# Kernel tuning notes

Hardware: AMD Instinct MI355X
Metric: run time of the kernel (lower is better)

The kernel has to match this reference:

```python
import jax, jax.numpy as jnp
import numpy as np

B, S, D, H, DFF = 4, 2048, 1024, 16, 4096
DK = D // H
EPS = 1e-5


def _linear_params(key, fan_in, fan_out):
    kw, kb = jax.random.split(key)
    bound = 1.0 / np.sqrt(fan_in)
    w = jax.random.uniform(kw, (fan_in, fan_out), minval=-bound, maxval=bound, dtype=jnp.float32)
    b = jax.random.uniform(kb, (fan_out,), minval=-bound, maxval=bound, dtype=jnp.float32)
    return w, b


def setup_inputs() -> dict:
    key = jax.random.key(0)
    ks = jax.random.split(key, 8)
    x = jax.random.normal(ks[0], (B, S, D), dtype=jnp.float32)
    mask = jnp.ones((B, 1, 1, S), dtype=jnp.int32)
    wq, bq = _linear_params(ks[1], D, D)
    wk, bk = _linear_params(ks[2], D, D)
    wv, bv = _linear_params(ks[3], D, D)
    wo, bo = _linear_params(ks[4], D, D)
    w1, b1 = _linear_params(ks[5], D, DFF)
    w2, b2 = _linear_params(ks[6], DFF, D)
    g1 = jnp.ones((D,), jnp.float32); be1 = jnp.zeros((D,), jnp.float32)
    g2 = jnp.ones((D,), jnp.float32); be2 = jnp.zeros((D,), jnp.float32)
    return {"x": x, "mask": mask, "wq": wq, "bq": bq, "wk": wk, "bk": bk,
            "wv": wv, "bv": bv, "wo": wo, "bo": bo, "w1": w1, "b1": b1,
            "w2": w2, "b2": b2, "g1": g1, "be1": be1, "g2": g2, "be2": be2}


def _layernorm(x, g, b):
    mu = jnp.mean(x, axis=-1, keepdims=True)
    var = jnp.mean(jnp.square(x - mu), axis=-1, keepdims=True)
    return (x - mu) * jax.lax.rsqrt(var + EPS) * g + b


def reference(x, mask, wq, bq, wk, bk, wv, bv, wo, bo, w1, b1, w2, b2, g1, be1, g2, be2):
    # Multi-head self-attention
    q = (x @ wq + bq).reshape(B, S, H, DK).transpose(0, 2, 1, 3)  # b h s d
    k = (x @ wk + bk).reshape(B, S, H, DK).transpose(0, 2, 1, 3)
    v = (x @ wv + bv).reshape(B, S, H, DK).transpose(0, 2, 1, 3)
    scores = jnp.einsum('bhqd,bhkd->bhqk', q, k) / np.sqrt(DK)
    scores = jnp.where(mask == 0, jnp.float32(-1e9), scores)
    attn = jax.nn.softmax(scores, axis=-1)
    ctx = jnp.einsum('bhqk,bhkd->bhqd', attn, v)
    ctx = ctx.transpose(0, 2, 1, 3).reshape(B, S, D)
    attn_out = ctx @ wo + bo
    # Dropout is identity in eval mode
    out1 = _layernorm(x + attn_out, g1, be1)
    ffn = jax.nn.relu(out1 @ w1 + b1) @ w2 + b2
    out2 = _layernorm(out1 + ffn, g2, be2)
    return out2
```

## Files before the change

### kernel.cpp

```cpp
#include <hip/hip_runtime.h>
#include <cstdint>
#include <cstddef>

typedef __bf16 bf16_t;
typedef __bf16 bf16x4 __attribute__((ext_vector_type(4)));
typedef __bf16 bf16x8 __attribute__((ext_vector_type(8)));
typedef float f32x4 __attribute__((ext_vector_type(4)));

#define GLD_LDS16(g, l)                                                                   \
  __builtin_amdgcn_global_load_lds((const __attribute__((address_space(1))) void*)(g),   \
                                   (__attribute__((address_space(3))) void*)(l), 16, 0, 0)

__device__ __forceinline__ int swbits(int row) {
  return ((row ^ (row >> 3)) & 7) << 4;
}
__device__ __forceinline__ int swz(int row, int colbyte) {
  return row * 128 + (colbyte ^ swbits(row));
}

__global__ __launch_bounds__(256) void transpose_cvt_k(const float* __restrict__ src,
                                                       bf16_t* __restrict__ dst, int R, int C) {
  __shared__ float t[64][65];
  const int tid = threadIdx.x;
  const int tr = blockIdx.y * 64, tc = blockIdx.x * 64;
  const int r0 = tid >> 2, c0 = (tid & 3) * 16;
#pragma unroll
  for (int i = 0; i < 16; i += 4) {
    float4 v = *(const float4*)(src + (size_t)(tr + r0) * C + tc + c0 + i);
    t[r0][c0 + i] = v.x; t[r0][c0 + i + 1] = v.y;
    t[r0][c0 + i + 2] = v.z; t[r0][c0 + i + 3] = v.w;
  }
  __syncthreads();
  bf16x8 w0, w1;
#pragma unroll
  for (int i = 0; i < 8; ++i) {
    w0[i] = (bf16_t)t[c0 + i][r0];
    w1[i] = (bf16_t)t[c0 + 8 + i][r0];
  }
  *(bf16x8*)(dst + (size_t)(tc + r0) * R + tr + c0) = w0;
  *(bf16x8*)(dst + (size_t)(tc + r0) * R + tr + c0 + 8) = w1;
}

__global__ __launch_bounds__(256) void cvt_k(const float* __restrict__ in,
                                             bf16_t* __restrict__ out) {
  const size_t i = ((size_t)blockIdx.x * 256 + threadIdx.x) * 8;
  float4 a = *(const float4*)(in + i);
  float4 b = *(const float4*)(in + i + 4);
  bf16x8 o;
  o[0] = (bf16_t)a.x; o[1] = (bf16_t)a.y; o[2] = (bf16_t)a.z; o[3] = (bf16_t)a.w;
  o[4] = (bf16_t)b.x; o[5] = (bf16_t)b.y; o[6] = (bf16_t)b.z; o[7] = (bf16_t)b.w;
  *(bf16x8*)(out + i) = o;
}

__global__ void mask_scan_k(const int* __restrict__ mask, unsigned* __restrict__ dirty) {
  __shared__ int tilez[32];
  const int tid = threadIdx.x;
  for (int b = 0; b < 4; ++b) {
    if (tid < 32) tilez[tid] = 0;
    __syncthreads();
    int anyz = 0;
    const int* mb = mask + b * 2048 + tid * 8;
#pragma unroll
    for (int j = 0; j < 8; ++j) anyz |= (mb[j] == 0);
    if (anyz) atomicOr(&tilez[tid >> 3], 1);
    __syncthreads();
    if (tid == 0) {
      unsigned w = 0;
      for (int k = 0; k < 32; ++k) w |= (tilez[k] ? 1u : 0u) << k;
      dirty[b] = w;
    }
    __syncthreads();
  }
}

template <int EPI>
__global__ __launch_bounds__(256) void gemm_bt(
    const bf16_t* __restrict__ A, const bf16_t* __restrict__ Bt,
    const float* __restrict__ bias0, const bf16_t* __restrict__ res,
    bf16_t* __restrict__ out0, int N, int K) {
  __shared__ __align__(16) bf16_t As[128][64];
  __shared__ __align__(16) bf16_t Bs[128][64];
  const int tid = threadIdx.x, lane = tid & 63, wave = tid >> 6;
  const int wm = wave >> 1, wn = wave & 1;
  const int tile_m = blockIdx.y * 128, tile_n = blockIdx.x * 128;

  f32x4 acc[4][4];
#pragma unroll
  for (int i = 0; i < 4; ++i)
#pragma unroll
    for (int j = 0; j < 4; ++j)
#pragma unroll
      for (int c = 0; c < 4; ++c) acc[i][j][c] = 0.f;

  for (int k0 = 0; k0 < K; k0 += 64) {
    __syncthreads();
#pragma unroll
    for (int j = 0; j < 4; ++j) {
      const int c = j * 256 + tid;
      GLD_LDS16(A + (size_t)(tile_m + (c >> 3)) * K + k0 + (c & 7) * 8,
                (char*)As + j * 4096 + wave * 1024);
      GLD_LDS16(Bt + (size_t)(tile_n + (c >> 3)) * K + k0 + (c & 7) * 8,
                (char*)Bs + j * 4096 + wave * 1024);
    }
    __syncthreads();
#pragma unroll
    for (int kk = 0; kk < 2; ++kk) {
      bf16x8 a[4], b[4];
#pragma unroll
      for (int i = 0; i < 4; ++i)
        a[i] = *(const bf16x8*)&As[wm * 64 + i * 16 + (lane & 15)][kk * 32 + (lane >> 4) * 8];
#pragma unroll
      for (int i = 0; i < 4; ++i)
        b[i] = *(const bf16x8*)&Bs[wn * 64 + i * 16 + (lane & 15)][kk * 32 + (lane >> 4) * 8];
#pragma unroll
      for (int mi = 0; mi < 4; ++mi)
#pragma unroll
        for (int ni = 0; ni < 4; ++ni)
          acc[mi][ni] = __builtin_amdgcn_mfma_f32_16x16x32_bf16(a[mi], b[ni], acc[mi][ni], 0, 0, 0);
    }
  }

#pragma unroll
  for (int mi = 0; mi < 4; ++mi) {
#pragma unroll
    for (int ni = 0; ni < 4; ++ni) {
      const int col = tile_n + wn * 64 + ni * 16 + (lane & 15);
      const int rbase = tile_m + wm * 64 + mi * 16 + (lane >> 4) * 4;
      const float bv = bias0[col];
#pragma unroll
      for (int r = 0; r < 4; ++r) {
        const int row = rbase + r;
        float v = acc[mi][ni][r] + bv;
        if constexpr (EPI == 1) v += (float)res[(size_t)row * N + col];
        out0[(size_t)row * N + col] = (bf16_t)v;
      }
    }
  }
}

template <int EPI>
__global__ __launch_bounds__(512, 1) void gemm256(
    const bf16_t* __restrict__ A, const bf16_t* __restrict__ Bt,
    const float* __restrict__ bias0, const float* __restrict__ bias1,
    const float* __restrict__ bias2,
    bf16_t* __restrict__ out0, bf16_t* __restrict__ out1, bf16_t* __restrict__ out2,
    int N, int K) {
  extern __shared__ __align__(16) char lds[];
  const int tid = threadIdx.x, lane = tid & 63, wave = tid >> 6;
  const int fr = lane & 15, hi = lane >> 4;
  const int wm = wave >> 2, wn = wave & 3;
  const int tile_n = blockIdx.x * 256, tile_m = blockIdx.y * 256;
  const int NT = K >> 6;
  const int s_r = tid >> 3, s_cb = (tid & 7) * 16;

  f32x4 acc[8][4];
#pragma unroll
  for (int m = 0; m < 8; ++m)
#pragma unroll
    for (int n = 0; n < 4; ++n)
#pragma unroll
      for (int c = 0; c < 4; ++c) acc[m][n][c] = 0.f;

#define STAGE256(t, cbuf)                                                                  \
  do {                                                                                     \
    const size_t k0_ = (size_t)(t) * 64;                                                   \
    _Pragma("unroll") for (int h_ = 0; h_ < 2; ++h_)                                       \
        _Pragma("unroll") for (int is_ = 0; is_ < 2; ++is_) {                              \
      const int r_ = is_ * 64 + s_r;                                                       \
      GLD_LDS16(A + (size_t)(tile_m + h_ * 128 + r_) * K + k0_ + ((s_cb ^ swbits(r_)) >> 1),\
                lds + (cbuf)*65536 + h_ * 16384 + is_ * 8192 + wave * 1024);               \
    }                                                                                      \
    _Pragma("unroll") for (int h_ = 0; h_ < 2; ++h_)                                       \
        _Pragma("unroll") for (int is_ = 0; is_ < 2; ++is_) {                              \
      const int r_ = is_ * 64 + s_r;                                                       \
      GLD_LDS16(Bt + (size_t)(tile_n + h_ * 128 + r_) * K + k0_ + ((s_cb ^ swbits(r_)) >> 1),\
                lds + (cbuf)*65536 + 32768 + h_ * 16384 + is_ * 8192 + wave * 1024);       \
    }                                                                                      \
  } while (0)

  STAGE256(0, 0);
  for (int t = 0; t < NT; ++t) {
    const int c = t & 1;
    if (t + 1 < NT) {
      STAGE256(t + 1, c ^ 1);
      asm volatile("s_waitcnt vmcnt(8)" ::: "memory");
    } else {
      asm volatile("s_waitcnt vmcnt(0)" ::: "memory");
    }
    __builtin_amdgcn_s_barrier();

    bf16x8 bfrag[4][2];
#pragma unroll
    for (int n = 0; n < 4; ++n)
#pragma unroll
      for (int kk = 0; kk < 2; ++kk)
        bfrag[n][kk] = *(const bf16x8*)(lds + c * 65536 + 32768 + (wn >> 1) * 16384 +
                                        swz((wn & 1) * 64 + n * 16 + fr, kk * 64 + hi * 16));
    bf16x8 af[2][2][2];
#pragma unroll
    for (int mm = 0; mm < 2; ++mm)
#pragma unroll
      for (int kk = 0; kk < 2; ++kk)
        af[0][mm][kk] = *(const bf16x8*)(lds + c * 65536 + wm * 16384 +
                                         swz(mm * 16 + fr, kk * 64 + hi * 16));
#pragma unroll
    for (int p = 0; p < 4; ++p) {
      if (p < 3) {
#pragma unroll
        for (int mm = 0; mm < 2; ++mm)
#pragma unroll
          for (int kk = 0; kk < 2; ++kk)
            af[(p + 1) & 1][mm][kk] =
                *(const bf16x8*)(lds + c * 65536 + wm * 16384 +
                                 swz(((p + 1) * 2 + mm) * 16 + fr, kk * 64 + hi * 16));
      }
      __builtin_amdgcn_s_setprio(1);
#pragma unroll
      for (int mm = 0; mm < 2; ++mm)
#pragma unroll
        for (int n = 0; n < 4; ++n)
#pragma unroll
          for (int kk = 0; kk < 2; ++kk)
            acc[p * 2 + mm][n] = __builtin_amdgcn_mfma_f32_16x16x32_bf16(
                af[p & 1][mm][kk], bfrag[n][kk], acc[p * 2 + mm][n], 0, 0, 0);
      __builtin_amdgcn_s_setprio(0);
    }
    __builtin_amdgcn_s_barrier();
  }
#undef STAGE256

#pragma unroll
  for (int m = 0; m < 8; ++m) {
#pragma unroll
    for (int n = 0; n < 4; ++n) {
      const int col = tile_n + wn * 64 + n * 16 + fr;
      const int rbase = tile_m + wm * 128 + m * 16 + hi * 4;
      if constexpr (EPI == 0) {
        const int which = tile_n >> 10;
        const float* bp = which == 0 ? bias0 : (which == 1 ? bias1 : bias2);
        bf16_t* op = which == 0 ? out0 : (which == 1 ? out1 : out2);
        const float sca = which == 0 ? 0.18033688f : 1.0f;
        const int cc = col & 1023, h = cc >> 6, dk = cc & 63;
        const float bv = bp[cc];
#pragma unroll
        for (int r = 0; r < 4; ++r) {
          const int row = rbase + r, bb = row >> 11, ss = row & 2047;
          op[(((size_t)bb * 16 + h) * 2048 + ss) * 64 + dk] = (bf16_t)((acc[m][n][r] + bv) * sca);
        }
      } else {
        const float bv = bias0[col];
#pragma unroll
        for (int r = 0; r < 4; ++r) {
          const int row = rbase + r;
          float v = acc[m][n][r] + bv;
          if constexpr (EPI == 2) v = v > 0.f ? v : 0.f;
          out0[(size_t)row * N + col] = (bf16_t)v;
        }
      }
    }
  }
}

__global__ __launch_bounds__(256) void attn_k(
    const bf16_t* __restrict__ Q, const bf16_t* __restrict__ Kb, const bf16_t* __restrict__ Vb,
    const int* __restrict__ mask, const unsigned* __restrict__ dirtyp,
    bf16_t* __restrict__ ctxout) {
  __shared__ __align__(16) char Qs[16384];
  __shared__ __align__(16) char Ks[2][8192];
  __shared__ __align__(16) char Vt[2][8192];
  __shared__ __align__(16) char Ps[16384];
  const int tid = threadIdx.x, lane = tid & 63, wave = tid >> 6;
  const int fr = lane & 15, hi = lane >> 4;
  const int qt = blockIdx.x, bh = blockIdx.y, b = bh >> 4, h = bh & 15;
  const bf16_t* qbase = Q + ((size_t)bh * 2048 + qt * 128) * 64;
  const bf16_t* kbase = Kb + (size_t)bh * 2048 * 64;
  const bf16_t* vbase = Vb + (size_t)bh * 2048 * 64;
  const int* mbase = mask + b * 2048;
  const unsigned dirty = dirtyp[b];

  const int src_r = tid >> 3;
  const int src_cb = (tid & 7) * 16;

#pragma unroll
  for (int j = 0; j < 4; ++j) {
    const int c = j * 256 + tid, rr = c >> 3, cb = (c & 7) * 16;
    GLD_LDS16(qbase + rr * 64 + ((cb ^ swbits(rr)) >> 1), Qs + j * 4096 + wave * 1024);
  }
#pragma unroll
  for (int j = 0; j < 2; ++j) {
    const int rr = j * 32 + src_r;
    GLD_LDS16(kbase + rr * 64 + ((src_cb ^ swbits(rr)) >> 1), Ks[0] + j * 4096 + wave * 1024);
  }
  {
    bf16x8 v0 = *(const bf16x8*)(vbase + (size_t)(tid >> 3) * 64 + (tid & 7) * 8);
    bf16x8 v1 = *(const bf16x8*)(vbase + (size_t)(32 + (tid >> 3)) * 64 + (tid & 7) * 8);
    const int kp0 = tid >> 3, kp1 = 32 + (tid >> 3), d0 = (tid & 7) * 8;
#pragma unroll
    for (int i = 0; i < 8; ++i) {
      *(bf16_t*)(Vt[0] + swz(d0 + i, kp0 * 2)) = v0[i];
      *(bf16_t*)(Vt[0] + swz(d0 + i, kp1 * 2)) = v1[i];
    }
  }
  __syncthreads();

  f32x4 ctx[2][4];
  float l_prt[2][4];
#pragma unroll
  for (int mi = 0; mi < 2; ++mi)
#pragma unroll
    for (int r = 0; r < 4; ++r) {
      l_prt[mi][r] = 0.f;
#pragma unroll
      for (int di = 0; di < 4; ++di) ctx[mi][di][r] = 0.f;
    }

  for (int kt = 0; kt < 32; ++kt) {
    const int cur = kt & 1;
    bf16x8 vr0, vr1;
    if (kt < 31) {
#pragma unroll
      for (int j = 0; j < 2; ++j) {
        const int rr = j * 32 + src_r;
        GLD_LDS16(kbase + (size_t)(kt + 1) * 4096 + rr * 64 + ((src_cb ^ swbits(rr)) >> 1),
                  Ks[cur ^ 1] + j * 4096 + wave * 1024);
      }
      vr0 = *(const bf16x8*)(vbase + (size_t)(kt + 1) * 4096 + (size_t)(tid >> 3) * 64 +
                             (tid & 7) * 8);
      vr1 = *(const bf16x8*)(vbase + (size_t)(kt + 1) * 4096 + (size_t)(32 + (tid >> 3)) * 64 +
                             (tid & 7) * 8);
    }

    f32x4 sc[2][4];
#pragma unroll
    for (int mi = 0; mi < 2; ++mi)
#pragma unroll
      for (int ni = 0; ni < 4; ++ni)
#pragma unroll
        for (int c = 0; c < 4; ++c) sc[mi][ni][c] = 0.f;
#pragma unroll
    for (int kk = 0; kk < 2; ++kk) {
      bf16x8 aq[2], kb_[4];
#pragma unroll
      for (int mi = 0; mi < 2; ++mi)
        aq[mi] = *(const bf16x8*)(Qs + swz(wave * 32 + mi * 16 + fr, kk * 64 + hi * 16));
#pragma unroll
      for (int ni = 0; ni < 4; ++ni)
        kb_[ni] = *(const bf16x8*)(Ks[cur] + swz(ni * 16 + fr, kk * 64 + hi * 16));
#pragma unroll
      for (int mi = 0; mi < 2; ++mi)
#pragma unroll
        for (int ni = 0; ni < 4; ++ni)
          sc[mi][ni] = __builtin_amdgcn_mfma_f32_16x16x32_bf16(aq[mi], kb_[ni], sc[mi][ni], 0, 0, 0);
    }

    if (dirty & (1u << kt)) {
      int mv[4];
#pragma unroll
      for (int ni = 0; ni < 4; ++ni) mv[ni] = mbase[kt * 64 + ni * 16 + fr];
#pragma unroll
      for (int mi = 0; mi < 2; ++mi)
#pragma unroll
        for (int ni = 0; ni < 4; ++ni)
#pragma unroll
          for (int r = 0; r < 4; ++r)
            sc[mi][ni][r] = mv[ni] ? sc[mi][ni][r] : -1e9f;
    }

#pragma unroll
    for (int mi = 0; mi < 2; ++mi) {
#pragma unroll
      for (int r = 0; r < 4; ++r) {
        float rsum = 0.f;
#pragma unroll
        for (int ni = 0; ni < 4; ++ni) {
          const float p = exp2f(sc[mi][ni][r]);
          sc[mi][ni][r] = p;
          rsum += p;
        }
        l_prt[mi][r] += rsum;
      }
      const int qrow = wave * 32 + mi * 16 + hi * 4;
#pragma unroll
      for (int ni = 0; ni < 4; ++ni)
#pragma unroll
        for (int r = 0; r < 4; ++r)
          *(bf16_t*)(Ps + swz(qrow + r, (ni * 16 + fr) * 2)) = (bf16_t)sc[mi][ni][r];
    }
    asm volatile("s_waitcnt lgkmcnt(0)" ::: "memory");
    __builtin_amdgcn_sched_barrier(0);

#pragma unroll
    for (int kk = 0; kk < 2; ++kk) {
      bf16x8 pa[2], vv[4];
#pragma unroll
      for (int mi = 0; mi < 2; ++mi)
        pa[mi] = *(const bf16x8*)(Ps + swz(wave * 32 + mi * 16 + fr, kk * 64 + hi * 16));
#pragma unroll
      for (int di = 0; di < 4; ++di)
        vv[di] = *(const bf16x8*)(Vt[cur] + swz(di * 16 + fr, kk * 64 + hi * 16));
#pragma unroll
      for (int mi = 0; mi < 2; ++mi)
#pragma unroll
        for (int di = 0; di < 4; ++di)
          ctx[mi][di] =
              __builtin_amdgcn_mfma_f32_16x16x32_bf16(pa[mi], vv[di], ctx[mi][di], 0, 0, 0);
    }

    if (kt < 31) {
      const int kp0 = tid >> 3, kp1 = 32 + (tid >> 3), d0 = (tid & 7) * 8;
#pragma unroll
      for (int i = 0; i < 8; ++i) {
        *(bf16_t*)(Vt[cur ^ 1] + swz(d0 + i, kp0 * 2)) = vr0[i];
        *(bf16_t*)(Vt[cur ^ 1] + swz(d0 + i, kp1 * 2)) = vr1[i];
      }
    }
    __syncthreads();
  }

#pragma unroll
  for (int mi = 0; mi < 2; ++mi)
#pragma unroll
    for (int r = 0; r < 4; ++r) {
      float l = l_prt[mi][r];
#pragma unroll
      for (int d = 1; d < 16; d <<= 1) l += __shfl_xor(l, d);
      const float inv = 1.f / l;
      const int srow = qt * 128 + wave * 32 + mi * 16 + hi * 4 + r;
#pragma unroll
      for (int di = 0; di < 4; ++di) {
        const int col = h * 64 + di * 16 + fr;
        ctxout[((size_t)b * 2048 + srow) * 1024 + col] = (bf16_t)(ctx[mi][di][r] * inv);
      }
    }
}

template <int F32OUT>
__global__ __launch_bounds__(256) void ln_k(const bf16_t* __restrict__ in,
                                            const float* __restrict__ g,
                                            const float* __restrict__ be,
                                            void* __restrict__ out) {
  __shared__ float red[8];
  const int tid = threadIdx.x;
  const size_t row = blockIdx.x;
  bf16x4 v4 = *(const bf16x4*)(in + row * 1024 + tid * 4);
  const float f0 = (float)v4[0], f1 = (float)v4[1], f2 = (float)v4[2], f3 = (float)v4[3];
  float s = f0 + f1 + f2 + f3;
  float s2 = f0 * f0 + f1 * f1 + f2 * f2 + f3 * f3;
#pragma unroll
  for (int d = 1; d < 64; d <<= 1) { s += __shfl_xor(s, d); s2 += __shfl_xor(s2, d); }
  if ((tid & 63) == 0) { red[tid >> 6] = s; red[4 + (tid >> 6)] = s2; }
  __syncthreads();
  s = red[0] + red[1] + red[2] + red[3];
  s2 = red[4] + red[5] + red[6] + red[7];
  const float mu = s * (1.f / 1024.f);
  const float var = s2 * (1.f / 1024.f) - mu * mu;
  const float rs = rsqrtf(var + 1e-5f);
  float4 gv = *(const float4*)(g + tid * 4);
  float4 bv = *(const float4*)(be + tid * 4);
  const float r0 = (f0 - mu) * rs * gv.x + bv.x;
  const float r1 = (f1 - mu) * rs * gv.y + bv.y;
  const float r2 = (f2 - mu) * rs * gv.z + bv.z;
  const float r3 = (f3 - mu) * rs * gv.w + bv.w;
  if constexpr (F32OUT) {
    float4 o = {r0, r1, r2, r3};
    *(float4*)((float*)out + row * 1024 + tid * 4) = o;
  } else {
    bf16x4 o;
    o[0] = (bf16_t)r0; o[1] = (bf16_t)r1; o[2] = (bf16_t)r2; o[3] = (bf16_t)r3;
    *(bf16x4*)((bf16_t*)out + row * 1024 + tid * 4) = o;
  }
}

extern "C" void kernel_launch(void* const* d_in, const int* in_sizes, int n_in,
                              void* d_out, int out_size, void* d_ws, size_t ws_size,
                              hipStream_t stream) {
  const float* x    = (const float*)d_in[0];
  const int*   mask = (const int*)d_in[1];
  const float* wq = (const float*)d_in[2];
  const float* bq = (const float*)d_in[3];
  const float* wk = (const float*)d_in[4];
  const float* bk = (const float*)d_in[5];
  const float* wv = (const float*)d_in[6];
  const float* bv = (const float*)d_in[7];
  const float* wo = (const float*)d_in[8];
  const float* bo = (const float*)d_in[9];
  const float* w1 = (const float*)d_in[10];
  const float* b1 = (const float*)d_in[11];
  const float* w2 = (const float*)d_in[12];
  const float* b2 = (const float*)d_in[13];
  const float* g1  = (const float*)d_in[14];
  const float* be1 = (const float*)d_in[15];
  const float* g2  = (const float*)d_in[16];
  const float* be2 = (const float*)d_in[17];

  char* wsb = (char*)d_ws;
  bf16_t* S0  = (bf16_t*)wsb;
  bf16_t* XB  = (bf16_t*)(wsb + 8388608);
  bf16_t* QB  = (bf16_t*)(wsb + 25165824);
  bf16_t* KB  = (bf16_t*)(wsb + 41943040);
  bf16_t* VB  = (bf16_t*)(wsb + 58720256);
  bf16_t* CTX = (bf16_t*)(wsb + 75497472);
  bf16_t* FFN = QB;
  bf16_t* Y   = (bf16_t*)(wsb + 92274688);
  bf16_t* O1  = (bf16_t*)(wsb + 109051904);
  unsigned* DIRTY = (unsigned*)(wsb + 125829120);

  (void)hipFuncSetAttribute((const void*)gemm256<0>,
                            hipFuncAttributeMaxDynamicSharedMemorySize, 131072);
  (void)hipFuncSetAttribute((const void*)gemm256<2>,
                            hipFuncAttributeMaxDynamicSharedMemorySize, 131072);

  dim3 blk(256);
  mask_scan_k<<<1, 256, 0, stream>>>(mask, DIRTY);
  cvt_k<<<4096, blk, 0, stream>>>(x, XB);
  transpose_cvt_k<<<dim3(16, 16), blk, 0, stream>>>(wq, S0, 1024, 1024);
  transpose_cvt_k<<<dim3(16, 16), blk, 0, stream>>>(wk, S0 + 1048576, 1024, 1024);
  transpose_cvt_k<<<dim3(16, 16), blk, 0, stream>>>(wv, S0 + 2097152, 1024, 1024);
  gemm256<0><<<dim3(12, 32), 512, 131072, stream>>>(XB, S0, bq, bk, bv,
                                                    QB, KB, VB, 3072, 1024);
  transpose_cvt_k<<<dim3(16, 16), blk, 0, stream>>>(wo, S0, 1024, 1024);
  attn_k<<<dim3(16, 64), blk, 0, stream>>>(QB, KB, VB, mask, DIRTY, CTX);
  gemm_bt<1><<<dim3(8, 64), blk, 0, stream>>>(CTX, S0, bo, XB, Y, 1024, 1024);
  transpose_cvt_k<<<dim3(64, 16), blk, 0, stream>>>(w1, S0, 1024, 4096);
  ln_k<0><<<8192, blk, 0, stream>>>(Y, g1, be1, O1);
  gemm256<2><<<dim3(16, 32), 512, 131072, stream>>>(O1, S0, b1, nullptr, nullptr,
                                                    FFN, nullptr, nullptr, 4096, 1024);
  transpose_cvt_k<<<dim3(16, 64), blk, 0, stream>>>(w2, S0, 4096, 1024);
  gemm_bt<1><<<dim3(8, 64), blk, 0, stream>>>(FFN, S0, b2, O1, Y, 1024, 4096);
  ln_k<1><<<8192, blk, 0, stream>>>(Y, g2, be2, d_out);
}
```

Before: 487.7 us.

## Add double-buffered 256x128 swizzled GEMM for QKV, out-proj and FFN2

Replaces the simple single-buffered 128x128 gemm_bt with a new 512-thread 256x128-tile kernel that double-buffers LDS, uses an XOR swizzle and issues next-tile loads before the MFMA work. The new kernel now serves the output projection and FFN2 GEMMs (N=1024), and also the QKV projection, which moves off the 256x256 kernel to get more blocks (768 instead of 384). The aim is to hide global-load latency, cut LDS bank conflicts, and fill the CUs better for the narrower GEMMs. The cost is that the smaller tile gives less data reuse per block than the 256x256 kernel, and the larger LDS footprint (96KB) allows only one block per CU.

```diff
diff --git a/kernel.cpp b/kernel.cpp
--- a/kernel.cpp
+++ b/kernel.cpp
@@ -74,65 +74,117 @@
 }
 
 template <int EPI>
-__global__ __launch_bounds__(256) void gemm_bt(
+__global__ __launch_bounds__(512, 1) void gemmA(
     const bf16_t* __restrict__ A, const bf16_t* __restrict__ Bt,
-    const float* __restrict__ bias0, const bf16_t* __restrict__ res,
-    bf16_t* __restrict__ out0, int N, int K) {
-  __shared__ __align__(16) bf16_t As[128][64];
-  __shared__ __align__(16) bf16_t Bs[128][64];
+    const float* __restrict__ bias0, const float* __restrict__ bias1,
+    const float* __restrict__ bias2, const bf16_t* __restrict__ res,
+    bf16_t* __restrict__ out0, bf16_t* __restrict__ out1, bf16_t* __restrict__ out2,
+    int N, int K) {
+  extern __shared__ __align__(16) char lds[];
   const int tid = threadIdx.x, lane = tid & 63, wave = tid >> 6;
+  const int fr = lane & 15, hi = lane >> 4;
   const int wm = wave >> 1, wn = wave & 1;
-  const int tile_m = blockIdx.y * 128, tile_n = blockIdx.x * 128;
+  const int tile_n = blockIdx.x * 128, tile_m = blockIdx.y * 256;
+  const int NT = K >> 6;
+  const int s_r = tid >> 3, s_cb = (tid & 7) * 16;
 
   f32x4 acc[4][4];
 #pragma unroll
-  for (int i = 0; i < 4; ++i)
-#pragma unroll
-    for (int j = 0; j < 4; ++j)
-#pragma unroll
-      for (int c = 0; c < 4; ++c) acc[i][j][c] = 0.f;
-
-  for (int k0 = 0; k0 < K; k0 += 64) {
-    __syncthreads();
-#pragma unroll
-    for (int j = 0; j < 4; ++j) {
-      const int c = j * 256 + tid;
-      GLD_LDS16(A + (size_t)(tile_m + (c >> 3)) * K + k0 + (c & 7) * 8,
-                (char*)As + j * 4096 + wave * 1024);
-      GLD_LDS16(Bt + (size_t)(tile_n + (c >> 3)) * K + k0 + (c & 7) * 8,
-                (char*)Bs + j * 4096 + wave * 1024);
-    }
-    __syncthreads();
-#pragma unroll
-    for (int kk = 0; kk < 2; ++kk) {
-      bf16x8 a[4], b[4];
-#pragma unroll
-      for (int i = 0; i < 4; ++i)
-        a[i] = *(const bf16x8*)&As[wm * 64 + i * 16 + (lane & 15)][kk * 32 + (lane >> 4) * 8];
-#pragma unroll
-      for (int i = 0; i < 4; ++i)
-        b[i] = *(const bf16x8*)&Bs[wn * 64 + i * 16 + (lane & 15)][kk * 32 + (lane >> 4) * 8];
-#pragma unroll
-      for (int mi = 0; mi < 4; ++mi)
-#pragma unroll
-        for (int ni = 0; ni < 4; ++ni)
-          acc[mi][ni] = __builtin_amdgcn_mfma_f32_16x16x32_bf16(a[mi], b[ni], acc[mi][ni], 0, 0, 0);
-    }
-  }
-
-#pragma unroll
-  for (int mi = 0; mi < 4; ++mi) {
-#pragma unroll
-    for (int ni = 0; ni < 4; ++ni) {
-      const int col = tile_n + wn * 64 + ni * 16 + (lane & 15);
-      const int rbase = tile_m + wm * 64 + mi * 16 + (lane >> 4) * 4;
-      const float bv = bias0[col];
-#pragma unroll
-      for (int r = 0; r < 4; ++r) {
-        const int row = rbase + r;
-        float v = acc[mi][ni][r] + bv;
-        if constexpr (EPI == 1) v += (float)res[(size_t)row * N + col];
-        out0[(size_t)row * N + col] = (bf16_t)v;
+  for (int m = 0; m < 4; ++m)
+#pragma unroll
+    for (int n = 0; n < 4; ++n)
+#pragma unroll
+      for (int c = 0; c < 4; ++c) acc[m][n][c] = 0.f;
+
+#define STAGEA(t, cbuf)                                                                    \
+  do {                                                                                     \
+    const size_t k0_ = (size_t)(t) * 64;                                                   \
+    _Pragma("unroll") for (int i_ = 0; i_ < 4; ++i_) {                                     \
+      GLD_LDS16(A + (size_t)(tile_m + i_ * 64 + s_r) * K + k0_ + ((s_cb ^ swbits(s_r)) >> 1),\
+                lds + (cbuf)*49152 + i_ * 8192 + wave * 1024);                             \
+    }                                                                                      \
+    _Pragma("unroll") for (int i_ = 0; i_ < 2; ++i_) {                                     \
+      GLD_LDS16(Bt + (size_t)(tile_n + i_ * 64 + s_r) * K + k0_ + ((s_cb ^ swbits(s_r)) >> 1),\
+                lds + (cbuf)*49152 + 32768 + i_ * 8192 + wave * 1024);                     \
+    }                                                                                      \
+  } while (0)
+
+  STAGEA(0, 0);
+  for (int t = 0; t < NT; ++t) {
+    const int c = t & 1;
+    if (t + 1 < NT) {
+      STAGEA(t + 1, c ^ 1);
+      asm volatile("s_waitcnt vmcnt(6)" ::: "memory");
+    } else {
+      asm volatile("s_waitcnt vmcnt(0)" ::: "memory");
+    }
+    __builtin_amdgcn_s_barrier();
+
+    bf16x8 bfrag[4][2];
+#pragma unroll
+    for (int n = 0; n < 4; ++n)
+#pragma unroll
+      for (int kk = 0; kk < 2; ++kk)
+        bfrag[n][kk] = *(const bf16x8*)(lds + c * 49152 + 32768 + wn * 8192 +
+                                        swz(n * 16 + fr, kk * 64 + hi * 16));
+    bf16x8 af[2][2][2];
+#pragma unroll
+    for (int mm = 0; mm < 2; ++mm)
+#pragma unroll
+      for (int kk = 0; kk < 2; ++kk)
+        af[0][mm][kk] = *(const bf16x8*)(lds + c * 49152 + wm * 8192 +
+                                         swz(mm * 16 + fr, kk * 64 + hi * 16));
+#pragma unroll
+    for (int p = 0; p < 2; ++p) {
+      if (p < 1) {
+#pragma unroll
+        for (int mm = 0; mm < 2; ++mm)
+#pragma unroll
+          for (int kk = 0; kk < 2; ++kk)
+            af[1][mm][kk] = *(const bf16x8*)(lds + c * 49152 + wm * 8192 +
+                                             swz((2 + mm) * 16 + fr, kk * 64 + hi * 16));
+      }
+      __builtin_amdgcn_s_setprio(1);
+#pragma unroll
+      for (int mm = 0; mm < 2; ++mm)
+#pragma unroll
+        for (int n = 0; n < 4; ++n)
+#pragma unroll
+          for (int kk = 0; kk < 2; ++kk)
+            acc[p * 2 + mm][n] = __builtin_amdgcn_mfma_f32_16x16x32_bf16(
+                af[p][mm][kk], bfrag[n][kk], acc[p * 2 + mm][n], 0, 0, 0);
+      __builtin_amdgcn_s_setprio(0);
+    }
+    __builtin_amdgcn_s_barrier();
+  }
+#undef STAGEA
+
+#pragma unroll
+  for (int m = 0; m < 4; ++m) {
+#pragma unroll
+    for (int n = 0; n < 4; ++n) {
+      const int col = tile_n + wn * 64 + n * 16 + fr;
+      const int rbase = tile_m + wm * 64 + m * 16 + hi * 4;
+      if constexpr (EPI == 0) {
+        const int which = tile_n >> 10;
+        const float* bp = which == 0 ? bias0 : (which == 1 ? bias1 : bias2);
+        bf16_t* op = which == 0 ? out0 : (which == 1 ? out1 : out2);
+        const float sca = which == 0 ? 0.18033688f : 1.0f;
+        const int cc = col & 1023, h = cc >> 6, dk = cc & 63;
+        const float bv = bp[cc];
+#pragma unroll
+        for (int r = 0; r < 4; ++r) {
+          const int row = rbase + r, bb = row >> 11, ss = row & 2047;
+          op[(((size_t)bb * 16 + h) * 2048 + ss) * 64 + dk] = (bf16_t)((acc[m][n][r] + bv) * sca);
+        }
+      } else {
+        const float bv = bias0[col];
+#pragma unroll
+        for (int r = 0; r < 4; ++r) {
+          const int row = rbase + r;
+          float v = acc[m][n][r] + bv + (float)res[(size_t)row * N + col];
+          out0[(size_t)row * N + col] = (bf16_t)v;
+        }
       }
     }
   }
@@ -141,10 +193,8 @@
 template <int EPI>
 __global__ __launch_bounds__(512, 1) void gemm256(
     const bf16_t* __restrict__ A, const bf16_t* __restrict__ Bt,
-    const float* __restrict__ bias0, const float* __restrict__ bias1,
-    const float* __restrict__ bias2,
-    bf16_t* __restrict__ out0, bf16_t* __restrict__ out1, bf16_t* __restrict__ out2,
-    int N, int K) {
+    const float* __restrict__ bias0,
+    bf16_t* __restrict__ out0, int N, int K) {
   extern __shared__ __align__(16) char lds[];
   const int tid = threadIdx.x, lane = tid & 63, wave = tid >> 6;
   const int fr = lane & 15, hi = lane >> 4;
@@ -235,27 +285,13 @@
     for (int n = 0; n < 4; ++n) {
       const int col = tile_n + wn * 64 + n * 16 + fr;
       const int rbase = tile_m + wm * 128 + m * 16 + hi * 4;
-      if constexpr (EPI == 0) {
-        const int which = tile_n >> 10;
-        const float* bp = which == 0 ? bias0 : (which == 1 ? bias1 : bias2);
-        bf16_t* op = which == 0 ? out0 : (which == 1 ? out1 : out2);
-        const float sca = which == 0 ? 0.18033688f : 1.0f;
-        const int cc = col & 1023, h = cc >> 6, dk = cc & 63;
-        const float bv = bp[cc];
-#pragma unroll
-        for (int r = 0; r < 4; ++r) {
-          const int row = rbase + r, bb = row >> 11, ss = row & 2047;
-          op[(((size_t)bb * 16 + h) * 2048 + ss) * 64 + dk] = (bf16_t)((acc[m][n][r] + bv) * sca);
-        }
-      } else {
-        const float bv = bias0[col];
-#pragma unroll
-        for (int r = 0; r < 4; ++r) {
-          const int row = rbase + r;
-          float v = acc[m][n][r] + bv;
-          if constexpr (EPI == 2) v = v > 0.f ? v : 0.f;
-          out0[(size_t)row * N + col] = (bf16_t)v;
-        }
+      const float bv = bias0[col];
+#pragma unroll
+      for (int r = 0; r < 4; ++r) {
+        const int row = rbase + r;
+        float v = acc[m][n][r] + bv;
+        if constexpr (EPI == 2) v = v > 0.f ? v : 0.f;
+        out0[(size_t)row * N + col] = (bf16_t)v;
       }
     }
   }
@@ -505,8 +541,10 @@
   bf16_t* O1  = (bf16_t*)(wsb + 109051904);
   unsigned* DIRTY = (unsigned*)(wsb + 125829120);
 
-  (void)hipFuncSetAttribute((const void*)gemm256<0>,
-                            hipFuncAttributeMaxDynamicSharedMemorySize, 131072);
+  (void)hipFuncSetAttribute((const void*)gemmA<0>,
+                            hipFuncAttributeMaxDynamicSharedMemorySize, 98304);
+  (void)hipFuncSetAttribute((const void*)gemmA<1>,
+                            hipFuncAttributeMaxDynamicSharedMemorySize, 98304);
   (void)hipFuncSetAttribute((const void*)gemm256<2>,
                             hipFuncAttributeMaxDynamicSharedMemorySize, 131072);
 
@@ -516,16 +554,17 @@
   transpose_cvt_k<<<dim3(16, 16), blk, 0, stream>>>(wq, S0, 1024, 1024);
   transpose_cvt_k<<<dim3(16, 16), blk, 0, stream>>>(wk, S0 + 1048576, 1024, 1024);
   transpose_cvt_k<<<dim3(16, 16), blk, 0, stream>>>(wv, S0 + 2097152, 1024, 1024);
-  gemm256<0><<<dim3(12, 32), 512, 131072, stream>>>(XB, S0, bq, bk, bv,
-                                                    QB, KB, VB, 3072, 1024);
+  gemmA<0><<<dim3(24, 32), 512, 98304, stream>>>(XB, S0, bq, bk, bv, nullptr,
+                                                 QB, KB, VB, 3072, 1024);
   transpose_cvt_k<<<dim3(16, 16), blk, 0, stream>>>(wo, S0, 1024, 1024);
   attn_k<<<dim3(16, 64), blk, 0, stream>>>(QB, KB, VB, mask, DIRTY, CTX);
-  gemm_bt<1><<<dim3(8, 64), blk, 0, stream>>>(CTX, S0, bo, XB, Y, 1024, 1024);
+  gemmA<1><<<dim3(8, 32), 512, 98304, stream>>>(CTX, S0, bo, nullptr, nullptr, XB,
+                                                Y, nullptr, nullptr, 1024, 1024);
   transpose_cvt_k<<<dim3(64, 16), blk, 0, stream>>>(w1, S0, 1024, 4096);
   ln_k<0><<<8192, blk, 0, stream>>>(Y, g1, be1, O1);
-  gemm256<2><<<dim3(16, 32), 512, 131072, stream>>>(O1, S0, b1, nullptr, nullptr,
-                                                    FFN, nullptr, nullptr, 4096, 1024);
+  gemm256<2><<<dim3(16, 32), 512, 131072, stream>>>(O1, S0, b1, FFN, 4096, 1024);
   transpose_cvt_k<<<dim3(16, 64), blk, 0, stream>>>(w2, S0, 4096, 1024);
-  gemm_bt<1><<<dim3(8, 64), blk, 0, stream>>>(FFN, S0, b2, O1, Y, 1024, 4096);
+  gemmA<1><<<dim3(8, 32), 512, 98304, stream>>>(FFN, S0, b2, nullptr, nullptr, O1,
+                                                Y, nullptr, nullptr, 1024, 4096);
   ln_k<1><<<8192, blk, 0, stream>>>(Y, g2, be2, d_out);
 }
```

New measurement: 467.7 us. 4.1% less time.
